# Kernel tuning notes

Hardware: AMD Instinct MI355X
Metric: run time of the kernel (lower is better)

The kernel has to match this reference:

```python
import jax, jax.numpy as jnp
import numpy as np

N = 100000
E = 1600000
B = 64
NUM_CLASSES = 10


def setup_inputs() -> dict:
    key = jax.random.key(0)
    ks = jax.random.split(key, 8)
    x = jax.random.normal(ks[0], (N, 5), dtype=jnp.float32)
    edge_index = jax.random.randint(ks[1], (2, E), 0, N, dtype=jnp.int64)
    batch = jnp.sort(jax.random.randint(ks[2], (N,), 0, B, dtype=jnp.int64))

    def glorot(k, fan_in, fan_out):
        s = jnp.sqrt(6.0 / (fan_in + fan_out)).astype(jnp.float32)
        return jax.random.uniform(k, (fan_in, fan_out), jnp.float32, -s, s)

    dims = [(5, 32), (32, 64), (64, 128), (128, 256)]
    Ws = [glorot(jax.random.fold_in(ks[3], i), a, b) for i, (a, b) in enumerate(dims)]
    bs = [jnp.zeros((b,), jnp.float32) for (_, b) in dims]
    fc1_w = glorot(ks[4], 256, 100)
    fc1_b = jnp.zeros((100,), jnp.float32)
    fc2_w = glorot(ks[5], 100, NUM_CLASSES)
    fc2_b = jnp.zeros((NUM_CLASSES,), jnp.float32)
    return {
        'x': x, 'edge_index': edge_index, 'batch': batch,
        'W1': Ws[0], 'b1': bs[0], 'W2': Ws[1], 'b2': bs[1],
        'W3': Ws[2], 'b3': bs[2], 'W4': Ws[3], 'b4': bs[3],
        'fc1_w': fc1_w, 'fc1_b': fc1_b, 'fc2_w': fc2_w, 'fc2_b': fc2_b,
    }


def _gcn_conv(x, W, b, src, dst, dinv):
    h = x @ W                                   # [N, out]
    norm = (dinv[src] * dinv[dst])[:, None]      # [E, 1]
    msg = h[src] * norm                          # gather + scale
    agg = jax.ops.segment_sum(msg, dst, num_segments=N)
    agg = agg + h * (dinv * dinv)[:, None]       # self-loop contribution
    return agg + b


def reference(x, edge_index, batch, W1, b1, W2, b2, W3, b3, W4, b4,
              fc1_w, fc1_b, fc2_w, fc2_b):
    src, dst = edge_index[0], edge_index[1]
    # degree including self-loop
    deg = jax.ops.segment_sum(jnp.ones((E,), jnp.float32), dst, num_segments=N) + 1.0
    dinv = jax.lax.rsqrt(deg)

    h = jax.nn.relu(_gcn_conv(x, W1, b1, src, dst, dinv))
    # mesh_unpool with pool target 0 -> identity
    h = jax.nn.relu(_gcn_conv(h, W2, b2, src, dst, dinv))
    h = jax.nn.relu(_gcn_conv(h, W3, b3, src, dst, dinv))
    h = jax.nn.relu(_gcn_conv(h, W4, b4, src, dst, dinv))

    # global mean pool over graphs
    sums = jax.ops.segment_sum(h, batch, num_segments=B)
    cnt = jax.ops.segment_sum(jnp.ones((N,), jnp.float32), batch, num_segments=B)
    pooled = sums / jnp.maximum(cnt, 1.0)[:, None]

    h = jax.nn.relu(pooled @ fc1_w + fc1_b)
    return jax.nn.log_softmax(h @ fc2_w + fc2_b, axis=-1)
```

## Files before the change

kernel.cpp:

```cpp
#include <hip/hip_runtime.h>
#include <hip/hip_bf16.h>
#include <cmath>

#define NN 100000
#define NE 1600000
#define NBATCH 64
#define NB 391
#define NBP 512
#define BCAP 5120
#define NPAD (NB * BCAP)

typedef __attribute__((ext_vector_type(8))) _Float16 f16x8;
typedef __attribute__((ext_vector_type(4))) float f32x4;
typedef __attribute__((ext_vector_type(2))) float f32x2;

__device__ __forceinline__ void atomAdd(float* p, float v) {
  unsafeAtomicAdd(p, v);
}

__device__ __forceinline__ unsigned char f2fp8(float f) {
  int pk = __builtin_amdgcn_cvt_pk_fp8_f32(f, f, 0, false);
  return (unsigned char)(pk & 0xff);
}

__device__ __forceinline__ void acc16(uint4 v, f32x2* acc) {
  acc[0] += __builtin_amdgcn_cvt_pk_f32_fp8(v.x, false);
  acc[1] += __builtin_amdgcn_cvt_pk_f32_fp8(v.x, true);
  acc[2] += __builtin_amdgcn_cvt_pk_f32_fp8(v.y, false);
  acc[3] += __builtin_amdgcn_cvt_pk_f32_fp8(v.y, true);
  acc[4] += __builtin_amdgcn_cvt_pk_f32_fp8(v.z, false);
  acc[5] += __builtin_amdgcn_cvt_pk_f32_fp8(v.z, true);
  acc[6] += __builtin_amdgcn_cvt_pk_f32_fp8(v.w, false);
  acc[7] += __builtin_amdgcn_cvt_pk_f32_fp8(v.w, true);
}

__global__ __launch_bounds__(256) void k_bin(const int* __restrict__ src,
    const int* __restrict__ dst, int* __restrict__ bucketCnt, unsigned* __restrict__ pairs,
    const float* __restrict__ W2, const float* __restrict__ W3, const float* __restrict__ W4,
    _Float16* __restrict__ Wt2, _Float16* __restrict__ Wt3, _Float16* __restrict__ Wt4) {
  __shared__ int hist[NBP];
  __shared__ int scn[NBP];
  __shared__ int ofs[NBP];
  __shared__ int gbase[NBP];
  __shared__ unsigned buf[4096];
  __shared__ unsigned short bufb[4096];
  const int base = blockIdx.x * 4096;
  const int n = (NE - base < 4096) ? NE - base : 4096;
  for (int i = threadIdx.x; i < NBP; i += 256) hist[i] = 0;
  __syncthreads();

  int myS[16], myD[16];
  int nloc = 0;
  for (int i = threadIdx.x, j = 0; i < n; i += 256, ++j) {
    myS[j] = src[base + i];
    myD[j] = dst[base + i];
    atomicAdd(&hist[myD[j] >> 8], 1);
    nloc = j + 1;
  }
  __syncthreads();

  scn[threadIdx.x] = hist[threadIdx.x];
  scn[threadIdx.x + 256] = hist[threadIdx.x + 256];
  __syncthreads();
  for (int off = 1; off < NBP; off <<= 1) {
    const int i0 = threadIdx.x, i1 = threadIdx.x + 256;
    int t0 = (i0 >= off) ? scn[i0 - off] : 0;
    int t1 = (i1 >= off) ? scn[i1 - off] : 0;
    __syncthreads();
    scn[i0] += t0;
    scn[i1] += t1;
    __syncthreads();
  }
  ofs[threadIdx.x] = scn[threadIdx.x] - hist[threadIdx.x];
  ofs[threadIdx.x + 256] = scn[threadIdx.x + 256] - hist[threadIdx.x + 256];
  for (int b = threadIdx.x; b < NB; b += 256) {
    int c = hist[b];
    if (c) gbase[b] = b * BCAP + atomicAdd(&bucketCnt[b], c);
  }
  __syncthreads();

  for (int j = 0; j < nloc; ++j) {
    int b = myD[j] >> 8;
    int slot = atomicAdd(&ofs[b], 1);
    buf[slot] = ((unsigned)myS[j] << 8) | ((unsigned)myD[j] & 255u);
    bufb[slot] = (unsigned short)b;
  }
  __syncthreads();

  for (int i = threadIdx.x; i < n; i += 256) {
    int b = (int)bufb[i];
    int ex = scn[b] - hist[b];
    pairs[gbase[b] + (i - ex)] = buf[i];
  }

  int idx = blockIdx.x * 256 + threadIdx.x;
  if (idx < 2048) {
    int k = idx / 64, m = idx - k * 64;
    Wt2[m * 32 + k] = (_Float16)W2[idx];
  } else if (idx < 10240) {
    int j = idx - 2048;
    int k = j / 128, m = j - k * 128;
    Wt3[m * 64 + k] = (_Float16)W3[j];
  } else if (idx < 43008) {
    int j = idx - 10240;
    int k = j / 256, m = j - k * 256;
    Wt4[m * 128 + k] = (_Float16)W4[j];
  }
}

__global__ __launch_bounds__(256) void k_cntfill(const unsigned* __restrict__ pairs,
    const int* __restrict__ bucketCnt, const int* __restrict__ batch,
    const float* __restrict__ x, int* __restrict__ rowbeg, int* __restrict__ rowend,
    float* __restrict__ dinv, int* __restrict__ csrc, float* __restrict__ pcnt,
    _Float16* __restrict__ xs8) {
  __shared__ int c[256];
  __shared__ int scn[256];
  __shared__ int rowb[256];
  __shared__ int ofs[256];
  __shared__ int h[64];
  const int tid = threadIdx.x;
  c[tid] = 0; ofs[tid] = 0;
  if (tid < 64) h[tid] = 0;
  __syncthreads();
  const int b = blockIdx.x;
  const int s = b * BCAP;
  const int e = s + bucketCnt[b];
  for (int i = s + tid; i < e; i += 256) atomicAdd(&c[pairs[i] & 255u], 1);
  __syncthreads();
  const int v = c[tid];
  scn[tid] = v;
  __syncthreads();
  for (int off = 1; off < 256; off <<= 1) {
    int t = (tid >= off) ? scn[tid - off] : 0;
    __syncthreads();
    scn[tid] += t;
    __syncthreads();
  }
  rowb[tid] = s + scn[tid] - v;
  const int node = b * 256 + tid;
  rowbeg[node] = rowb[tid];
  rowend[node] = rowb[tid] + v;
  if (node < NN) {
    const float di = rsqrtf((float)v + 1.0f);
    dinv[node] = di;
    f16x8 o = {0, 0, 0, 0, 0, 0, 0, 0};
    o[0] = (_Float16)(x[(size_t)node * 5 + 0] * di);
    o[1] = (_Float16)(x[(size_t)node * 5 + 1] * di);
    o[2] = (_Float16)(x[(size_t)node * 5 + 2] * di);
    o[3] = (_Float16)(x[(size_t)node * 5 + 3] * di);
    o[4] = (_Float16)(x[(size_t)node * 5 + 4] * di);
    *(f16x8*)(xs8 + (size_t)node * 8) = o;
    atomicAdd(&h[batch[node]], 1);
  }
  __syncthreads();
  for (int i = s + tid; i < e; i += 256) {
    unsigned p = pairs[i];
    int t = (int)(p & 255u);
    int pos = rowb[t] + atomicAdd(&ofs[t], 1);
    csrc[pos] = (int)(p >> 8);
  }
  if (tid < 64 && h[tid]) atomAdd(&pcnt[tid], (float)h[tid]);
}

struct MegaArgs {
  const _Float16* xs8;
  const int* rowbeg; const int* rowend; const int* csrc;
  const float* dinv;
  const float* W1; const float* b1;
  unsigned char* F0;
  const _Float16* Wt2; const float* b2;
  unsigned char* F1;
  const _Float16* Wt3; const float* b3;
  unsigned char* F2;
  const _Float16* Wt4; const float* b4;
  const int* batch; float* pooled; const float* pcnt;
  const float* fc1w; const float* fc1b; const float* fc2w; const float* fc2b;
  float* out;
};

__global__ __launch_bounds__(256) void kw_l1(MegaArgs a) {
  __shared__ float w_s[160];
  __shared__ float b_s[32];
  const int tid = threadIdx.x;
  if (tid < 160) w_s[tid] = a.W1[tid];
  if (tid < 32) b_s[tid] = a.b1[tid];
  __syncthreads();
  const int r = blockIdx.x * 256 + tid;
  if (r >= NN) return;
  const float di = a.dinv[r];
  f16x8 av = *(const f16x8*)(a.xs8 + (size_t)r * 8);
  f16x8 a1 = {0, 0, 0, 0, 0, 0, 0, 0};
  f16x8 a2 = {0, 0, 0, 0, 0, 0, 0, 0};
  f16x8 a3 = {0, 0, 0, 0, 0, 0, 0, 0};
  int e = a.rowbeg[r];
  const int e1 = a.rowend[r];
  for (; e + 4 <= e1; e += 4) {
    const int s0 = a.csrc[e], s1 = a.csrc[e + 1], s2 = a.csrc[e + 2], s3 = a.csrc[e + 3];
    av += *(const f16x8*)(a.xs8 + (size_t)s0 * 8);
    a1 += *(const f16x8*)(a.xs8 + (size_t)s1 * 8);
    a2 += *(const f16x8*)(a.xs8 + (size_t)s2 * 8);
    a3 += *(const f16x8*)(a.xs8 + (size_t)s3 * 8);
  }
  for (; e < e1; ++e) av += *(const f16x8*)(a.xs8 + (size_t)a.csrc[e] * 8);
  a2 += a3;
  av += a1;
  av += a2;
  const float f0 = (float)av[0] * di, f1 = (float)av[1] * di, f2 = (float)av[2] * di,
              f3 = (float)av[3] * di, f4 = (float)av[4] * di;
  float v[32];
#pragma unroll
  for (int j = 0; j < 32; ++j) {
    float s = b_s[j] + f0 * w_s[j] + f1 * w_s[32 + j] + f2 * w_s[64 + j]
                     + f3 * w_s[96 + j] + f4 * w_s[128 + j];
    v[j] = fmaxf(s, 0.f) * di;
  }
  unsigned u[8];
#pragma unroll
  for (int g2 = 0; g2 < 8; ++g2) {
    int uu = 0;
    uu = __builtin_amdgcn_cvt_pk_fp8_f32(v[4 * g2],     v[4 * g2 + 1], uu, false);
    uu = __builtin_amdgcn_cvt_pk_fp8_f32(v[4 * g2 + 2], v[4 * g2 + 3], uu, true);
    u[g2] = (unsigned)uu;
  }
  uint4* op = (uint4*)(a.F0 + (size_t)r * 32);
  op[0] = make_uint4(u[0], u[1], u[2], u[3]);
  op[1] = make_uint4(u[4], u[5], u[6], u[7]);
}

template<int K, int M, int MODE>
__global__ __launch_bounds__(256) void kw_fgemm(MegaArgs a,
    const unsigned char* __restrict__ in,
    const _Float16* __restrict__ Wt, const float* __restrict__ bias,
    unsigned char* __restrict__ outp) {
  constexpr int KC = 32;
  constexpr int KP = K + 8;
  constexpr int CTW = M / 64;
  constexpr int TPR = K / 16;
  constexpr int RPP = 256 / TPR;
  constexpr int NPASS = (64 + RPP - 1) / RPP;
  __shared__ _Float16 a_s[64 * KP];
  const int tid = threadIdx.x;
  const int wave = tid >> 6, lane = tid & 63;
  const int m16 = lane & 15, q = lane >> 4;
  const int r0 = blockIdx.x * 64;

  {
    const int rowg = tid / TPR;
    const int c = (tid % TPR) * 16;
    const unsigned char* bp = in + c;
#pragma unroll
    for (int pass = 0; pass < NPASS; ++pass) {
      const int row = pass * RPP + rowg;
      if (row < 64) {
        const int r = r0 + row;
        f32x2 acc8[8];
#pragma unroll
        for (int i = 0; i < 8; ++i) acc8[i] = (f32x2){0.f, 0.f};
        float di = 0.f;
        if (r < NN) {
          di = a.dinv[r];
          acc16(*(const uint4*)(bp + (size_t)r * K), acc8);
          int e = a.rowbeg[r];
          const int e1 = a.rowend[r];
          for (; e + 4 <= e1; e += 4) {
            const int s0 = a.csrc[e],     s1 = a.csrc[e + 1];
            const int s2 = a.csrc[e + 2], s3 = a.csrc[e + 3];
            const uint4 v0 = *(const uint4*)(bp + (size_t)s0 * K);
            const uint4 v1 = *(const uint4*)(bp + (size_t)s1 * K);
            const uint4 v2 = *(const uint4*)(bp + (size_t)s2 * K);
            const uint4 v3 = *(const uint4*)(bp + (size_t)s3 * K);
            acc16(v0, acc8); acc16(v1, acc8); acc16(v2, acc8); acc16(v3, acc8);
          }
          for (; e < e1; ++e)
            acc16(*(const uint4*)(bp + (size_t)a.csrc[e] * K), acc8);
        }
        _Float16 h[16];
#pragma unroll
        for (int i = 0; i < 8; ++i) {
          h[2 * i]     = (_Float16)(acc8[i].x * di);
          h[2 * i + 1] = (_Float16)(acc8[i].y * di);
        }
        *(uint4*)&a_s[row * KP + c]     = *(uint4*)&h[0];
        *(uint4*)&a_s[row * KP + c + 8] = *(uint4*)&h[8];
      }
    }
  }
  __syncthreads();

  f32x4 acc[4][CTW];
#pragma unroll
  for (int rt = 0; rt < 4; ++rt)
#pragma unroll
    for (int ct = 0; ct < CTW; ++ct) acc[rt][ct] = (f32x4){0.f, 0.f, 0.f, 0.f};

  const _Float16* wp = Wt + (size_t)(wave * (M / 4)) * K + q * 8;
#pragma unroll
  for (int kc = 0; kc < K; kc += KC) {
    f16x8 bfr[CTW];
#pragma unroll
    for (int ct = 0; ct < CTW; ++ct)
      bfr[ct] = *(const f16x8*)(wp + (size_t)(ct * 16 + m16) * K + kc);
#pragma unroll
    for (int rt = 0; rt < 4; ++rt) {
      f16x8 afr = *(const f16x8*)&a_s[(rt * 16 + m16) * KP + kc + q * 8];
#pragma unroll
      for (int ct = 0; ct < CTW; ++ct)
        acc[rt][ct] = __builtin_amdgcn_mfma_f32_16x16x32_f16(afr, bfr[ct], acc[rt][ct], 0, 0, 0);
    }
  }

  if constexpr (MODE == 1) {
    const int rlast = (r0 + 63 < NN) ? r0 + 63 : NN - 1;
    const int bmin = a.batch[r0];
    const int bmax = a.batch[rlast];
    int rowb[4][4];
#pragma unroll
    for (int rt = 0; rt < 4; ++rt)
#pragma unroll
      for (int reg = 0; reg < 4; ++reg) {
        const int row = r0 + rt * 16 + q * 4 + reg;
        rowb[rt][reg] = (row < NN) ? a.batch[row] : -1;
      }
#pragma unroll
    for (int ct = 0; ct < CTW; ++ct) {
      const int col = wave * (M / 4) + ct * 16 + m16;
      const float bv = bias[col];
      for (int b = bmin; b <= bmax; ++b) {
        float s = 0.f;
#pragma unroll
        for (int rt = 0; rt < 4; ++rt)
#pragma unroll
          for (int reg = 0; reg < 4; ++reg)
            if (rowb[rt][reg] == b) s += fmaxf(acc[rt][ct][reg] + bv, 0.f);
        s += __shfl_xor(s, 16);
        s += __shfl_xor(s, 32);
        if (q == 0) atomAdd(&a.pooled[b * M + col], s);
      }
    }
  } else {
    float dsc[4][4];
#pragma unroll
    for (int rt = 0; rt < 4; ++rt)
#pragma unroll
      for (int reg = 0; reg < 4; ++reg) {
        const int row = r0 + rt * 16 + q * 4 + reg;
        dsc[rt][reg] = (row < NN) ? a.dinv[row] : 0.f;
      }
#pragma unroll
    for (int rt = 0; rt < 4; ++rt) {
#pragma unroll
      for (int ct = 0; ct < CTW; ++ct) {
        const int col = wave * (M / 4) + ct * 16 + m16;
        const float bv = bias[col];
#pragma unroll
        for (int reg = 0; reg < 4; ++reg) {
          const int row = r0 + rt * 16 + q * 4 + reg;
          if (row < NN) {
            float vv = fmaxf(acc[rt][ct][reg] + bv, 0.f) * dsc[rt][reg];
            outp[(size_t)row * M + col] = f2fp8(vv);
          }
        }
      }
    }
  }
}

__global__ __launch_bounds__(256) void kw_mlp(MegaArgs a) {
  __shared__ float p[256];
  __shared__ float h1[100];
  __shared__ float lo[10];
  const int tid = threadIdx.x;
  const int b = blockIdx.x;
  const float inv = 1.0f / fmaxf(a.pcnt[b], 1.0f);
  p[tid] = a.pooled[b * 256 + tid] * inv;
  __syncthreads();
  for (int j = tid; j < 100; j += 256) {
    float s = a.fc1b[j];
    for (int k = 0; k < 256; ++k) s += p[k] * a.fc1w[k * 100 + j];
    h1[j] = fmaxf(s, 0.f);
  }
  __syncthreads();
  if (tid < 10) {
    float s = a.fc2b[tid];
    for (int k = 0; k < 100; ++k) s += h1[k] * a.fc2w[k * 10 + tid];
    lo[tid] = s;
  }
  __syncthreads();
  if (tid == 0) {
    float m = lo[0];
    for (int j = 1; j < 10; ++j) m = fmaxf(m, lo[j]);
    float ssum = 0.f;
    for (int j = 0; j < 10; ++j) ssum += expf(lo[j] - m);
    float lse = m + logf(ssum);
    for (int j = 0; j < 10; ++j) a.out[b * 10 + j] = lo[j] - lse;
  }
}

extern "C" void kernel_launch(void* const* d_in, const int* in_sizes, int n_in,
                              void* d_out, int out_size, void* d_ws, size_t ws_size,
                              hipStream_t stream) {
  const float* x     = (const float*)d_in[0];
  const int*   ei    = (const int*)d_in[1];
  const int*   batch = (const int*)d_in[2];
  const float* W1 = (const float*)d_in[3];  const float* b1 = (const float*)d_in[4];
  const float* W2 = (const float*)d_in[5];  const float* b2 = (const float*)d_in[6];
  const float* W3 = (const float*)d_in[7];  const float* b3 = (const float*)d_in[8];
  const float* W4 = (const float*)d_in[9];  const float* b4 = (const float*)d_in[10];
  const float* fc1w = (const float*)d_in[11]; const float* fc1b = (const float*)d_in[12];
  const float* fc2w = (const float*)d_in[13]; const float* fc2b = (const float*)d_in[14];
  float* out = (float*)d_out;

  const int* src = ei;
  const int* dst = ei + NE;

  float* ws = (float*)d_ws;
  float* pooled = ws;
  float* pcnt   = pooled + 16384;
  int*   bucketCnt = (int*)(pcnt + 64);
  float* dinv   = (float*)(bucketCnt + 512);
  int*   rowbeg = (int*)(dinv + 100352);
  int*   rowend = rowbeg + 100352;
  int*   csrc   = rowend + 100352;
  unsigned* pairs = (unsigned*)(csrc + NPAD);
  _Float16* xs8 = (_Float16*)(pairs + NPAD);
  unsigned char* F0 = (unsigned char*)(xs8 + 800768);
  unsigned char* F1 = F0 + 3200000;
  unsigned char* F2 = F1 + 6400000;
  _Float16* Wt2 = (_Float16*)(F2 + 12800000);
  _Float16* Wt3 = Wt2 + 32 * 64;
  _Float16* Wt4 = Wt3 + 64 * 128;

  (void)hipMemsetAsync(pooled, 0, (16384 + 64 + 512) * sizeof(float), stream);
  k_bin<<<(NE + 4095) / 4096, 256, 0, stream>>>(src, dst, bucketCnt, pairs,
                                                W2, W3, W4, Wt2, Wt3, Wt4);
  k_cntfill<<<NB, 256, 0, stream>>>(pairs, bucketCnt, batch, x,
                                    rowbeg, rowend, dinv, csrc, pcnt, xs8);

  MegaArgs m;
  m.xs8 = xs8; m.rowbeg = rowbeg; m.rowend = rowend; m.csrc = csrc;
  m.dinv = dinv;
  m.W1 = W1; m.b1 = b1; m.F0 = F0;
  m.Wt2 = Wt2; m.b2 = b2; m.F1 = F1;
  m.Wt3 = Wt3; m.b3 = b3; m.F2 = F2;
  m.Wt4 = Wt4; m.b4 = b4;
  m.batch = batch; m.pooled = pooled; m.pcnt = pcnt;
  m.fc1w = fc1w; m.fc1b = fc1b; m.fc2w = fc2w; m.fc2b = fc2b;
  m.out = out;

  kw_l1<<<(NN + 255) / 256, 256, 0, stream>>>(m);
  kw_fgemm<32, 64, 0><<<(NN + 63) / 64, 256, 0, stream>>>(m, F0, Wt2, b2, F1);
  kw_fgemm<64, 128, 0><<<(NN + 63) / 64, 256, 0, stream>>>(m, F1, Wt3, b3, F2);
  kw_fgemm<128, 256, 1><<<(NN + 63) / 64, 256, 0, stream>>>(m, F2, Wt4, b4, nullptr);
  kw_mlp<<<NBATCH, 256, 0, stream>>>(m);
}
```

Before: 280.9 us.

## Pad CSR rows to multiples of four and gather with vectorized index loads

```diff
diff --git a/kernel.cpp b/kernel.cpp
--- a/kernel.cpp
+++ b/kernel.cpp
@@ -7,7 +7,7 @@
 #define NBATCH 64
 #define NB 391
 #define NBP 512
-#define BCAP 5120
+#define BCAP 6144
 #define NPAD (NB * BCAP)
 
 typedef __attribute__((ext_vector_type(8))) _Float16 f16x8;
@@ -112,7 +112,8 @@
     const int* __restrict__ bucketCnt, const int* __restrict__ batch,
     const float* __restrict__ x, int* __restrict__ rowbeg, int* __restrict__ rowend,
     float* __restrict__ dinv, int* __restrict__ csrc, float* __restrict__ pcnt,
-    _Float16* __restrict__ xs8) {
+    _Float16* __restrict__ xs8, unsigned char* __restrict__ F0,
+    unsigned char* __restrict__ F1, unsigned char* __restrict__ F2) {
   __shared__ int c[256];
   __shared__ int scn[256];
   __shared__ int rowb[256];
@@ -128,7 +129,8 @@
   for (int i = s + tid; i < e; i += 256) atomicAdd(&c[pairs[i] & 255u], 1);
   __syncthreads();
   const int v = c[tid];
-  scn[tid] = v;
+  const int pv = (v + 3) & ~3;
+  scn[tid] = pv;
   __syncthreads();
   for (int off = 1; off < 256; off <<= 1) {
     int t = (tid >= off) ? scn[tid - off] : 0;
@@ -136,10 +138,11 @@
     scn[tid] += t;
     __syncthreads();
   }
-  rowb[tid] = s + scn[tid] - v;
+  rowb[tid] = s + scn[tid] - pv;
   const int node = b * 256 + tid;
   rowbeg[node] = rowb[tid];
   rowend[node] = rowb[tid] + v;
+  for (int p = v; p < pv; ++p) csrc[rowb[tid] + p] = NN;
   if (node < NN) {
     const float di = rsqrtf((float)v + 1.0f);
     dinv[node] = di;
@@ -151,6 +154,13 @@
     o[4] = (_Float16)(x[(size_t)node * 5 + 4] * di);
     *(f16x8*)(xs8 + (size_t)node * 8) = o;
     atomicAdd(&h[batch[node]], 1);
+  }
+  if (b == 0 && tid < 15) {
+    const uint4 z = make_uint4(0u, 0u, 0u, 0u);
+    if (tid < 1)      ((uint4*)(xs8 + (size_t)NN * 8))[tid] = z;
+    else if (tid < 3) ((uint4*)(F0 + (size_t)NN * 32))[tid - 1] = z;
+    else if (tid < 7) ((uint4*)(F1 + (size_t)NN * 64))[tid - 3] = z;
+    else              ((uint4*)(F2 + (size_t)NN * 128))[tid - 7] = z;
   }
   __syncthreads();
   for (int i = s + tid; i < e; i += 256) {
@@ -188,23 +198,37 @@
   const int r = blockIdx.x * 256 + tid;
   if (r >= NN) return;
   const float di = a.dinv[r];
-  f16x8 av = *(const f16x8*)(a.xs8 + (size_t)r * 8);
-  f16x8 a1 = {0, 0, 0, 0, 0, 0, 0, 0};
-  f16x8 a2 = {0, 0, 0, 0, 0, 0, 0, 0};
-  f16x8 a3 = {0, 0, 0, 0, 0, 0, 0, 0};
-  int e = a.rowbeg[r];
-  const int e1 = a.rowend[r];
-  for (; e + 4 <= e1; e += 4) {
-    const int s0 = a.csrc[e], s1 = a.csrc[e + 1], s2 = a.csrc[e + 2], s3 = a.csrc[e + 3];
-    av += *(const f16x8*)(a.xs8 + (size_t)s0 * 8);
-    a1 += *(const f16x8*)(a.xs8 + (size_t)s1 * 8);
-    a2 += *(const f16x8*)(a.xs8 + (size_t)s2 * 8);
-    a3 += *(const f16x8*)(a.xs8 + (size_t)s3 * 8);
-  }
-  for (; e < e1; ++e) av += *(const f16x8*)(a.xs8 + (size_t)a.csrc[e] * 8);
-  a2 += a3;
-  av += a1;
-  av += a2;
+  const _Float16* xs = a.xs8;
+  f16x8 av = *(const f16x8*)(xs + (size_t)r * 8);
+  f16x8 a0 = {0,0,0,0,0,0,0,0}, a1 = {0,0,0,0,0,0,0,0};
+  f16x8 a2 = {0,0,0,0,0,0,0,0}, a3 = {0,0,0,0,0,0,0,0};
+  const int eb = a.rowbeg[r];
+  const int nIt = (a.rowend[r] - eb + 3) >> 2;
+  const uint4* cp = (const uint4*)(a.csrc + eb);
+  uint4 i0 = cp[0], i1 = cp[1];
+  int it = 0;
+  for (; it + 2 <= nIt; it += 2) {
+    const f16x8 f0 = *(const f16x8*)(xs + (size_t)i0.x * 8);
+    const f16x8 f1 = *(const f16x8*)(xs + (size_t)i0.y * 8);
+    const f16x8 f2 = *(const f16x8*)(xs + (size_t)i0.z * 8);
+    const f16x8 f3 = *(const f16x8*)(xs + (size_t)i0.w * 8);
+    const f16x8 f4 = *(const f16x8*)(xs + (size_t)i1.x * 8);
+    const f16x8 f5 = *(const f16x8*)(xs + (size_t)i1.y * 8);
+    const f16x8 f6 = *(const f16x8*)(xs + (size_t)i1.z * 8);
+    const f16x8 f7 = *(const f16x8*)(xs + (size_t)i1.w * 8);
+    const uint4 n0 = cp[it + 2], n1 = cp[it + 3];
+    a0 += f0; a1 += f1; a2 += f2; a3 += f3;
+    a0 += f4; a1 += f5; a2 += f6; a3 += f7;
+    i0 = n0; i1 = n1;
+  }
+  if (it < nIt) {
+    const f16x8 f0 = *(const f16x8*)(xs + (size_t)i0.x * 8);
+    const f16x8 f1 = *(const f16x8*)(xs + (size_t)i0.y * 8);
+    const f16x8 f2 = *(const f16x8*)(xs + (size_t)i0.z * 8);
+    const f16x8 f3 = *(const f16x8*)(xs + (size_t)i0.w * 8);
+    a0 += f0; a1 += f1; a2 += f2; a3 += f3;
+  }
+  a0 += a1; a2 += a3; a0 += a2; av += a0;
   const float f0 = (float)av[0] * di, f1 = (float)av[1] * di, f2 = (float)av[2] * di,
               f3 = (float)av[3] * di, f4 = (float)av[4] * di;
   float v[32];
@@ -227,17 +251,19 @@
   op[1] = make_uint4(u[4], u[5], u[6], u[7]);
 }
 
-template<int K, int M, int MODE>
-__global__ __launch_bounds__(256) void kw_fgemm(MegaArgs a,
+template<int K, int M, int MODE, int THREADS>
+__global__ __launch_bounds__(THREADS) void kw_fgemm(MegaArgs a,
     const unsigned char* __restrict__ in,
     const _Float16* __restrict__ Wt, const float* __restrict__ bias,
     unsigned char* __restrict__ outp) {
   constexpr int KC = 32;
   constexpr int KP = K + 8;
-  constexpr int CTW = M / 64;
+  constexpr int NW = THREADS / 64;
+  constexpr int MW = M / NW;
+  constexpr int CTW = MW / 16;
   constexpr int TPR = K / 16;
-  constexpr int RPP = 256 / TPR;
-  constexpr int NPASS = (64 + RPP - 1) / RPP;
+  constexpr int RPP = THREADS / TPR;
+  constexpr int NPASS = 64 / RPP;
   __shared__ _Float16 a_s[64 * KP];
   const int tid = threadIdx.x;
   const int wave = tid >> 6, lane = tid & 63;
@@ -251,38 +277,49 @@
 #pragma unroll
     for (int pass = 0; pass < NPASS; ++pass) {
       const int row = pass * RPP + rowg;
-      if (row < 64) {
-        const int r = r0 + row;
-        f32x2 acc8[8];
-#pragma unroll
-        for (int i = 0; i < 8; ++i) acc8[i] = (f32x2){0.f, 0.f};
-        float di = 0.f;
-        if (r < NN) {
-          di = a.dinv[r];
-          acc16(*(const uint4*)(bp + (size_t)r * K), acc8);
-          int e = a.rowbeg[r];
-          const int e1 = a.rowend[r];
-          for (; e + 4 <= e1; e += 4) {
-            const int s0 = a.csrc[e],     s1 = a.csrc[e + 1];
-            const int s2 = a.csrc[e + 2], s3 = a.csrc[e + 3];
-            const uint4 v0 = *(const uint4*)(bp + (size_t)s0 * K);
-            const uint4 v1 = *(const uint4*)(bp + (size_t)s1 * K);
-            const uint4 v2 = *(const uint4*)(bp + (size_t)s2 * K);
-            const uint4 v3 = *(const uint4*)(bp + (size_t)s3 * K);
-            acc16(v0, acc8); acc16(v1, acc8); acc16(v2, acc8); acc16(v3, acc8);
-          }
-          for (; e < e1; ++e)
-            acc16(*(const uint4*)(bp + (size_t)a.csrc[e] * K), acc8);
+      const int r = r0 + row;
+      f32x2 acc8[8];
+#pragma unroll
+      for (int i = 0; i < 8; ++i) acc8[i] = (f32x2){0.f, 0.f};
+      float di = 0.f;
+      if (r < NN) {
+        di = a.dinv[r];
+        const int eb = a.rowbeg[r];
+        const int nIt = (a.rowend[r] - eb + 3) >> 2;
+        const uint4* cp = (const uint4*)(a.csrc + eb);
+        uint4 i0 = cp[0], i1 = cp[1];
+        acc16(*(const uint4*)(bp + (size_t)r * K), acc8);
+        int it = 0;
+        for (; it + 2 <= nIt; it += 2) {
+          const uint4 f0 = *(const uint4*)(bp + (size_t)i0.x * K);
+          const uint4 f1 = *(const uint4*)(bp + (size_t)i0.y * K);
+          const uint4 f2 = *(const uint4*)(bp + (size_t)i0.z * K);
+          const uint4 f3 = *(const uint4*)(bp + (size_t)i0.w * K);
+          const uint4 f4 = *(const uint4*)(bp + (size_t)i1.x * K);
+          const uint4 f5 = *(const uint4*)(bp + (size_t)i1.y * K);
+          const uint4 f6 = *(const uint4*)(bp + (size_t)i1.z * K);
+          const uint4 f7 = *(const uint4*)(bp + (size_t)i1.w * K);
+          const uint4 n0 = cp[it + 2], n1 = cp[it + 3];
+          acc16(f0, acc8); acc16(f1, acc8); acc16(f2, acc8); acc16(f3, acc8);
+          acc16(f4, acc8); acc16(f5, acc8); acc16(f6, acc8); acc16(f7, acc8);
+          i0 = n0; i1 = n1;
         }
-        _Float16 h[16];
-#pragma unroll
-        for (int i = 0; i < 8; ++i) {
-          h[2 * i]     = (_Float16)(acc8[i].x * di);
-          h[2 * i + 1] = (_Float16)(acc8[i].y * di);
+        if (it < nIt) {
+          const uint4 f0 = *(const uint4*)(bp + (size_t)i0.x * K);
+          const uint4 f1 = *(const uint4*)(bp + (size_t)i0.y * K);
+          const uint4 f2 = *(const uint4*)(bp + (size_t)i0.z * K);
+          const uint4 f3 = *(const uint4*)(bp + (size_t)i0.w * K);
+          acc16(f0, acc8); acc16(f1, acc8); acc16(f2, acc8); acc16(f3, acc8);
         }
-        *(uint4*)&a_s[row * KP + c]     = *(uint4*)&h[0];
-        *(uint4*)&a_s[row * KP + c + 8] = *(uint4*)&h[8];
-      }
+      }
+      _Float16 h[16];
+#pragma unroll
+      for (int i = 0; i < 8; ++i) {
+        h[2 * i]     = (_Float16)(acc8[i].x * di);
+        h[2 * i + 1] = (_Float16)(acc8[i].y * di);
+      }
+      *(uint4*)&a_s[row * KP + c]     = *(uint4*)&h[0];
+      *(uint4*)&a_s[row * KP + c + 8] = *(uint4*)&h[8];
     }
   }
   __syncthreads();
@@ -293,7 +330,7 @@
 #pragma unroll
     for (int ct = 0; ct < CTW; ++ct) acc[rt][ct] = (f32x4){0.f, 0.f, 0.f, 0.f};
 
-  const _Float16* wp = Wt + (size_t)(wave * (M / 4)) * K + q * 8;
+  const _Float16* wp = Wt + (size_t)(wave * MW) * K + q * 8;
 #pragma unroll
   for (int kc = 0; kc < K; kc += KC) {
     f16x8 bfr[CTW];
@@ -323,7 +360,7 @@
       }
 #pragma unroll
     for (int ct = 0; ct < CTW; ++ct) {
-      const int col = wave * (M / 4) + ct * 16 + m16;
+      const int col = wave * MW + ct * 16 + m16;
       const float bv = bias[col];
       for (int b = bmin; b <= bmax; ++b) {
         float s = 0.f;
@@ -350,7 +387,7 @@
     for (int rt = 0; rt < 4; ++rt) {
 #pragma unroll
       for (int ct = 0; ct < CTW; ++ct) {
-        const int col = wave * (M / 4) + ct * 16 + m16;
+        const int col = wave * MW + ct * 16 + m16;
         const float bv = bias[col];
 #pragma unroll
         for (int reg = 0; reg < 4; ++reg) {
@@ -424,9 +461,9 @@
   unsigned* pairs = (unsigned*)(csrc + NPAD);
   _Float16* xs8 = (_Float16*)(pairs + NPAD);
   unsigned char* F0 = (unsigned char*)(xs8 + 800768);
-  unsigned char* F1 = F0 + 3200000;
-  unsigned char* F2 = F1 + 6400000;
-  _Float16* Wt2 = (_Float16*)(F2 + 12800000);
+  unsigned char* F1 = F0 + 3200128;
+  unsigned char* F2 = F1 + 6400128;
+  _Float16* Wt2 = (_Float16*)(F2 + 12800128);
   _Float16* Wt3 = Wt2 + 32 * 64;
   _Float16* Wt4 = Wt3 + 64 * 128;
 
@@ -434,7 +471,8 @@
   k_bin<<<(NE + 4095) / 4096, 256, 0, stream>>>(src, dst, bucketCnt, pairs,
                                                 W2, W3, W4, Wt2, Wt3, Wt4);
   k_cntfill<<<NB, 256, 0, stream>>>(pairs, bucketCnt, batch, x,
-                                    rowbeg, rowend, dinv, csrc, pcnt, xs8);
+                                    rowbeg, rowend, dinv, csrc, pcnt, xs8,
+                                    F0, F1, F2);
 
   MegaArgs m;
   m.xs8 = xs8; m.rowbeg = rowbeg; m.rowend = rowend; m.csrc = csrc;
@@ -447,9 +485,10 @@
   m.fc1w = fc1w; m.fc1b = fc1b; m.fc2w = fc2w; m.fc2b = fc2b;
   m.out = out;
 
+  const int gtile = (NN + 63) / 64;
   kw_l1<<<(NN + 255) / 256, 256, 0, stream>>>(m);
-  kw_fgemm<32, 64, 0><<<(NN + 63) / 64, 256, 0, stream>>>(m, F0, Wt2, b2, F1);
-  kw_fgemm<64, 128, 0><<<(NN + 63) / 64, 256, 0, stream>>>(m, F1, Wt3, b3, F2);
-  kw_fgemm<128, 256, 1><<<(NN + 63) / 64, 256, 0, stream>>>(m, F2, Wt4, b4, nullptr);
+  kw_fgemm<32, 64, 0, 128><<<gtile, 128, 0, stream>>>(m, F0, Wt2, b2, F1);
+  kw_fgemm<64, 128, 0, 256><<<gtile, 256, 0, stream>>>(m, F1, Wt3, b3, F2);
+  kw_fgemm<128, 256, 1, 256><<<gtile, 256, 0, stream>>>(m, F2, Wt4, b4, nullptr);
   kw_mlp<<<NBATCH, 256, 0, stream>>>(m);
 }
```

Result: no change. 277.5 us (-1.2%).
